# Performance work log

Hardware: AMD Instinct MI355X
Metric: run time of the kernel (lower is better)

The kernel has to match this reference:

```python
import jax, jax.numpy as jnp
import numpy as np

B = 262144
N_MAX = 4
N_EXPERTS = sum(n * n for n in range(1, N_MAX + 1))  # 30
# offset of expert block for each n (experts within n indexed by l*l + l + m)
OFFSETS = np.cumsum([0] + [n * n for n in range(1, N_MAX)])  # [0,1,5,14]


def _expert_id(n, l, m):
    off = jnp.asarray(OFFSETS, dtype=jnp.int32)
    return off[n - 1] + l * l + l + m  # (B,) int


def setup_inputs() -> dict:
    key = jax.random.key(0)
    ks = jax.random.split(key, 12)
    x = jax.random.normal(ks[0], (B, 3), dtype=jnp.float32)
    # valid coupled quantum numbers: 1<=n<=4, 0<=l<n, -l<=m<=l
    n = jax.random.randint(ks[1], (B,), 1, N_MAX + 1)
    ul = jax.random.uniform(ks[2], (B,))
    l = jnp.floor(ul * n.astype(jnp.float32)).astype(jnp.int32)
    l = jnp.clip(l, 0, n - 1)
    um = jax.random.uniform(ks[3], (B,))
    m = jnp.floor(um * (2 * l + 1).astype(jnp.float32)).astype(jnp.int32) - l
    m = jnp.clip(m, -l, l)
    s = 0.1
    W0 = jax.random.normal(ks[4], (3, 128), dtype=jnp.float32) * s
    b0 = jnp.zeros((128,), dtype=jnp.float32)
    W1 = jax.random.normal(ks[5], (128, 64), dtype=jnp.float32) * s
    b1 = jnp.zeros((64,), dtype=jnp.float32)
    Wa = jax.random.normal(ks[6], (N_EXPERTS, 64, 32), dtype=jnp.float32) * s
    ba = jax.random.normal(ks[7], (N_EXPERTS, 32), dtype=jnp.float32) * s
    Wb = jax.random.normal(ks[8], (N_EXPERTS, 32, 2), dtype=jnp.float32) * s
    bb = jax.random.normal(ks[9], (N_EXPERTS, 2), dtype=jnp.float32) * s
    return {"x": x, "n": n.astype(jnp.int32), "l": l, "m": m,
            "W0": W0, "b0": b0, "W1": W1, "b1": b1,
            "Wa": Wa, "ba": ba, "Wb": Wb, "bb": bb}


def reference(x, n, l, m, W0, b0, W1, b1, Wa, ba, Wb, bb):
    eid = _expert_id(n, l, m)  # (B,)
    # shared trunk (dropout is identity in eval mode)
    h = jnp.tanh(x @ W0 + b0)          # (B,128)
    h = jnp.tanh(h @ W1 + b1)          # (B,64)
    # per-sample expert dispatch via irregular gather of tiny MLP weights
    g = jnp.tanh(jnp.einsum('bd,bdh->bh', h, Wa[eid]) + ba[eid])  # (B,32)
    psi = jnp.einsum('bh,bho->bo', g, Wb[eid]) + bb[eid]          # (B,2)
    norm = jnp.sqrt(jnp.sum(psi * psi, axis=1, keepdims=True) + 1e-6)
    return psi / norm
```

## Files before the change

### kernel.cpp

```cpp
#include <hip/hip_runtime.h>
#include <math.h>


#define THREADS 64
#define NE 30
#define HB 256
#define PER 1024
#define MAXBLK 4126
#define SA 67
#define SG 36

typedef short bf16x8 __attribute__((ext_vector_type(8)));
typedef float f32x4 __attribute__((ext_vector_type(4)));

__device__ __forceinline__ int expert_id(int nn, int ll, int mm) {
    return ((nn - 1) * nn * (2 * nn - 1)) / 6 + ll * ll + ll + mm;
}

__device__ __forceinline__ float fast_tanh(float v) {
    float e = __builtin_exp2f(v * 2.885390082f);
    return fmaf(-2.0f, __builtin_amdgcn_rcpf(e + 1.0f), 1.0f);
}

__device__ __forceinline__ unsigned int f2b(float f) {
    unsigned int u = __float_as_uint(f);
    return (u + 0x7fffu + ((u >> 16) & 1u)) >> 16;
}
__device__ __forceinline__ float b2f(unsigned int b) {
    return __uint_as_float(b << 16);
}
__device__ __forceinline__ unsigned int packsplit(float v) {
    const unsigned int hb = f2b(v);
    const float lo = v - b2f(hb);
    return (__float_as_uint(lo) & 0xffff0000u) | hb;
}

union U8 { unsigned int u[4]; bf16x8 v; };
__device__ __forceinline__ void unpack8(const unsigned int* w, bf16x8& hi, bf16x8& lo) {
    U8 H, L;
#pragma unroll
    for (int i = 0; i < 4; ++i) {
        H.u[i] = __builtin_amdgcn_perm(w[2 * i + 1], w[2 * i], 0x05040100u);
        L.u[i] = __builtin_amdgcn_perm(w[2 * i + 1], w[2 * i], 0x07060302u);
    }
    hi = H.v; lo = L.v;
}

__global__ void hist_pack_kernel(const int* __restrict__ nq, const int* __restrict__ lq,
                                 const int* __restrict__ mq,
                                 int* __restrict__ eidr, int* __restrict__ cnt,
                                 const float* __restrict__ W1,
                                 unsigned short* __restrict__ W1fh, unsigned short* __restrict__ W1fl,
                                 const float* __restrict__ Wa,
                                 unsigned short* __restrict__ Wafh, unsigned short* __restrict__ Wafl,
                                 int B) {
    const int tid = threadIdx.x;
    const int bx = blockIdx.x;
    if (bx < HB) {
        __shared__ int h[NE];
        if (tid < NE) h[tid] = 0;
        __syncthreads();
        const int base = bx * PER;
        for (int i = tid; i < PER; i += blockDim.x) {
            const int e = expert_id(nq[base + i], lq[base + i], mq[base + i]);
            const int r = atomicAdd(&h[e], 1);
            eidr[base + i] = (r << 5) | e;
        }
        __syncthreads();
        if (tid < NE) cnt[bx * NE + tid] = h[tid];
    } else if (bx == HB) {
        for (int i = tid; i < 8192; i += blockDim.x) {
            const int j = i & 7, s = (i >> 3) & 15, q = (i >> 7) & 3;
            const int nt = (i >> 9) & 3, c = i >> 11;
            const int k = c * 32 + q * 8 + j, n = nt * 16 + s;
            const float w = W1[k * 64 + n];
            const unsigned int hb = f2b(w);
            W1fh[i] = (unsigned short)hb;
            W1fl[i] = (unsigned short)f2b(w - b2f(hb));
        }
    } else {
        const int e = bx - HB - 1;
        for (int i = tid; i < 2048; i += blockDim.x) {
            const int j = i & 7, s = (i >> 3) & 15, q = (i >> 7) & 3;
            const int nt2 = (i >> 9) & 1, c2 = (i >> 10) & 1;
            const int d = c2 * 32 + q * 8 + j, hh = nt2 * 16 + s;
            const float w = Wa[e * 2048 + d * 32 + hh];
            const unsigned int hb = f2b(w);
            Wafh[e * 2048 + i] = (unsigned short)hb;
            Wafl[e * 2048 + i] = (unsigned short)f2b(w - b2f(hb));
        }
    }
}

__global__ void scatter_kernel(const int* __restrict__ eidr, const int* __restrict__ cnt,
                               int* __restrict__ perm, int4* __restrict__ desc) {
    __shared__ int cl[HB * NE];
    __shared__ int bb[NE], tq[NE], esrt[NE + 1];
    const int tid = threadIdx.x;
    const int bx = blockIdx.x;
    for (int i = tid; i < HB * NE; i += blockDim.x) cl[i] = cnt[i];
    __syncthreads();
    if (tid < NE) {
        int s = 0, mybase = 0;
#pragma unroll 4
        for (int blk = 0; blk < HB; ++blk) {
            if (blk == bx) mybase = s;
            s += cl[blk * NE + tid];
        }
        bb[tid] = mybase;
        tq[tid] = s;
    }
    __syncthreads();
    if (tid == 0) {
        int es = 0;
        for (int e = 0; e < NE; ++e) { esrt[e] = es; es += tq[e]; }
        esrt[NE] = es;
    }
    __syncthreads();

    if (bx == HB) {
        __shared__ int pb[NE + 1];
        if (tid == 0) {
            int c = 0;
            for (int e = 0; e < NE; ++e) { pb[e] = c; c += (tq[e] + THREADS - 1) >> 6; }
            pb[NE] = c;
        }
        __syncthreads();
        const int tot = pb[NE];
        for (int b = tid; b < MAXBLK; b += blockDim.x) {
            int4 d = make_int4(-1, 0, 0, 0);
            if (b < tot) {
                int e = 0;
                while (pb[e + 1] <= b) ++e;
                const int seg = b - pb[e];
                d.x = e;
                d.y = esrt[e] + (seg << 6);
                d.z = min(THREADS, tq[e] - (seg << 6));
            }
            desc[b] = d;
        }
        return;
    }

    const int base = bx * PER;
    for (int i = tid; i < PER; i += blockDim.x) {
        const int p = eidr[base + i];
        const int e = p & 31;
        perm[esrt[e] + bb[e] + (p >> 5)] = base + i;
    }
}

__global__ __launch_bounds__(THREADS, 4) void wfc_kernel(
    const float* __restrict__ x, const int* __restrict__ perm,
    const int4* __restrict__ desc,
    const float* __restrict__ W0, const float* __restrict__ b0,
    const bf16x8* __restrict__ W1fh, const bf16x8* __restrict__ W1fl,
    const float* __restrict__ b1,
    const bf16x8* __restrict__ Wafh, const bf16x8* __restrict__ Wafl,
    const float* __restrict__ ba,
    const float* __restrict__ Wb, const float* __restrict__ bb,
    float* __restrict__ out)
{
    __shared__ unsigned int sbuf[2304];

    const int4 dsc = desc[blockIdx.x];
    if (dsc.x < 0) return;
    const int eid  = __builtin_amdgcn_readfirstlane(dsc.x);
    const int start = dsc.y;
    const int cnt   = dsc.z;

    const int tid = threadIdx.x;
    const bool valid = tid < cnt;
    const int idx = perm[start + (valid ? tid : 0)];

    const int lane = tid & 63;
    const int wv   = tid >> 6;
    const int qd   = lane >> 4;
    const int l16  = lane & 15;

    const float x0 = x[idx * 3 + 0];
    const float x1 = x[idx * 3 + 1];
    const float x2 = x[idx * 3 + 2];

    f32x4 acc[4][4];
#pragma unroll
    for (int nt = 0; nt < 4; ++nt) {
        const float bv = b1[nt * 16 + l16];
#pragma unroll
        for (int mt = 0; mt < 4; ++mt) {
            f32x4 c; c[0] = bv; c[1] = bv; c[2] = bv; c[3] = bv;
            acc[mt][nt] = c;
        }
    }

    for (int c = 0; c < 4; ++c) {
        if (c) __syncthreads();
#pragma unroll
        for (int kk = 0; kk < 32; ++kk) {
            const int k = c * 32 + kk;
            const float pre = fmaf(x0, W0[k], fmaf(x1, W0[128 + k], fmaf(x2, W0[256 + k], b0[k])));
            sbuf[kk * SA + tid] = packsplit(fast_tanh(pre));
        }
        __syncthreads();

        bf16x8 Bhi[4], Blo[4];
#pragma unroll
        for (int nt = 0; nt < 4; ++nt) {
            const int rec = (c * 4 + nt) * 64 + qd * 16 + l16;
            Bhi[nt] = W1fh[rec];
            Blo[nt] = W1fl[rec];
        }
#pragma unroll
        for (int mt = 0; mt < 4; ++mt) {
            unsigned int a[8];
            const int mrow = wv * 64 + mt * 16 + l16;
#pragma unroll
            for (int j = 0; j < 8; ++j) a[j] = sbuf[(qd * 8 + j) * SA + mrow];
            bf16x8 Ahi, Alo;
            unpack8(a, Ahi, Alo);
#pragma unroll
            for (int nt = 0; nt < 4; ++nt) {
                acc[mt][nt] = __builtin_amdgcn_mfma_f32_16x16x32_bf16(Ahi, Bhi[nt], acc[mt][nt], 0, 0, 0);
                acc[mt][nt] = __builtin_amdgcn_mfma_f32_16x16x32_bf16(Ahi, Blo[nt], acc[mt][nt], 0, 0, 0);
                acc[mt][nt] = __builtin_amdgcn_mfma_f32_16x16x32_bf16(Alo, Bhi[nt], acc[mt][nt], 0, 0, 0);
            }
        }
    }

    f32x4 acc2[4][2];
#pragma unroll
    for (int nt2 = 0; nt2 < 2; ++nt2) {
        const float bv = ba[(eid << 5) + nt2 * 16 + l16];
#pragma unroll
        for (int mt = 0; mt < 4; ++mt) {
            f32x4 c; c[0] = bv; c[1] = bv; c[2] = bv; c[3] = bv;
            acc2[mt][nt2] = c;
        }
    }

    const bf16x8* __restrict__ waeh = Wafh + (eid << 8);
    const bf16x8* __restrict__ wael = Wafl + (eid << 8);
    for (int c2 = 0; c2 < 2; ++c2) {
        __syncthreads();
#pragma unroll
        for (int mt = 0; mt < 4; ++mt) {
#pragma unroll
            for (int ntl = 0; ntl < 2; ++ntl) {
#pragma unroll
                for (int r = 0; r < 4; ++r) {
                    const float h2 = fast_tanh(acc[mt][c2 * 2 + ntl][r]);
                    const int dl  = ntl * 16 + l16;
                    const int row = wv * 64 + mt * 16 + qd * 4 + r;
                    sbuf[dl * SA + row] = packsplit(h2);
                }
            }
        }
        __syncthreads();

        bf16x8 B2hi[2], B2lo[2];
#pragma unroll
        for (int nt2 = 0; nt2 < 2; ++nt2) {
            const int rec = (c2 * 2 + nt2) * 64 + qd * 16 + l16;
            B2hi[nt2] = waeh[rec];
            B2lo[nt2] = wael[rec];
        }
#pragma unroll
        for (int mt = 0; mt < 4; ++mt) {
            unsigned int a[8];
            const int mrow = wv * 64 + mt * 16 + l16;
#pragma unroll
            for (int j = 0; j < 8; ++j) a[j] = sbuf[(qd * 8 + j) * SA + mrow];
            bf16x8 Ahi, Alo;
            unpack8(a, Ahi, Alo);
#pragma unroll
            for (int nt2 = 0; nt2 < 2; ++nt2) {
                acc2[mt][nt2] = __builtin_amdgcn_mfma_f32_16x16x32_bf16(Ahi, B2hi[nt2], acc2[mt][nt2], 0, 0, 0);
                acc2[mt][nt2] = __builtin_amdgcn_mfma_f32_16x16x32_bf16(Ahi, B2lo[nt2], acc2[mt][nt2], 0, 0, 0);
                acc2[mt][nt2] = __builtin_amdgcn_mfma_f32_16x16x32_bf16(Alo, B2hi[nt2], acc2[mt][nt2], 0, 0, 0);
            }
        }
    }

    __syncthreads();
    float* g2 = (float*)sbuf;
#pragma unroll
    for (int mt = 0; mt < 4; ++mt) {
#pragma unroll
        for (int nt2 = 0; nt2 < 2; ++nt2) {
#pragma unroll
            for (int r = 0; r < 4; ++r) {
                const int row = wv * 64 + mt * 16 + qd * 4 + r;
                g2[row * SG + nt2 * 16 + l16] = fast_tanh(acc2[mt][nt2][r]);
            }
        }
    }
    __syncthreads();

    float gv[32];
    {
        const float4* grow = (const float4*)(g2 + tid * SG);
#pragma unroll
        for (int i = 0; i < 8; ++i) {
            float4 v = grow[i];
            gv[4 * i + 0] = v.x; gv[4 * i + 1] = v.y;
            gv[4 * i + 2] = v.z; gv[4 * i + 3] = v.w;
        }
    }

    const float* __restrict__ wbe = Wb + (eid << 6);
    float p0 = bb[2 * eid], p1 = bb[2 * eid + 1];
#pragma unroll
    for (int h = 0; h < 32; ++h) {
        p0 = fmaf(gv[h], wbe[2 * h + 0], p0);
        p1 = fmaf(gv[h], wbe[2 * h + 1], p1);
    }

    const float s = fmaf(p0, p0, fmaf(p1, p1, 1e-6f));
    const float inv = 1.0f / sqrtf(s);
    if (valid) {
        float2 o; o.x = p0 * inv; o.y = p1 * inv;
        ((float2*)out)[idx] = o;
    }
}

extern "C" void kernel_launch(void* const* d_in, const int* in_sizes, int n_in,
                              void* d_out, int out_size, void* d_ws, size_t ws_size,
                              hipStream_t stream) {
    const float* x  = (const float*)d_in[0];
    const int*   n  = (const int*)d_in[1];
    const int*   l  = (const int*)d_in[2];
    const int*   m  = (const int*)d_in[3];
    const float* W0 = (const float*)d_in[4];
    const float* b0 = (const float*)d_in[5];
    const float* W1 = (const float*)d_in[6];
    const float* b1 = (const float*)d_in[7];
    const float* Wa = (const float*)d_in[8];
    const float* ba = (const float*)d_in[9];
    const float* Wb = (const float*)d_in[10];
    const float* bb = (const float*)d_in[11];
    float* out = (float*)d_out;

    const int B = in_sizes[1];

    int*            perm  = (int*)d_ws;
    int*            eidr  = perm + B;
    int*            cnt   = eidr + B;
    int4*           desc  = (int4*)(cnt + HB * NE);
    unsigned short* W1fh  = (unsigned short*)(desc + MAXBLK);
    unsigned short* W1fl  = W1fh + 8192;
    unsigned short* Wafh  = W1fl + 8192;
    unsigned short* Wafl  = Wafh + NE * 2048;

    hist_pack_kernel<<<HB + 1 + NE, 256, 0, stream>>>(
        n, l, m, eidr, cnt, W1, W1fh, W1fl, Wa, Wafh, Wafl, B);
    scatter_kernel<<<HB + 1, 256, 0, stream>>>(eidr, cnt, perm, desc);
    wfc_kernel<<<MAXBLK, THREADS, 0, stream>>>(
        x, perm, desc, W0, b0,
        (const bf16x8*)W1fh, (const bf16x8*)W1fl, b1,
        (const bf16x8*)Wafh, (const bf16x8*)Wafl, ba, Wb, bb, out);
}
```

Baseline: 156.8 us.

## Fuse histogram and scatter into one kernel with a grid-wide spin barrier

Merges the histogram and scatter kernels into one prologue kernel. Blocks publish their per-expert counts and then spin on a global atomic counter until all 256 histogram blocks have arrived. Each block keeps its packed ranks in registers instead of writing them to global memory and reading them back. The per-block descriptor table is dropped, and each main-kernel block now finds its expert segment by scanning the 30 expert totals. This removes one kernel launch and a global round trip, but relies on all 256 blocks being co-resident and adds a memset plus per-block scan work.

```diff
diff --git a/kernel.cpp b/kernel.cpp
--- a/kernel.cpp
+++ b/kernel.cpp
@@ -46,28 +46,78 @@
     hi = H.v; lo = L.v;
 }
 
-__global__ void hist_pack_kernel(const int* __restrict__ nq, const int* __restrict__ lq,
-                                 const int* __restrict__ mq,
-                                 int* __restrict__ eidr, int* __restrict__ cnt,
-                                 const float* __restrict__ W1,
-                                 unsigned short* __restrict__ W1fh, unsigned short* __restrict__ W1fl,
-                                 const float* __restrict__ Wa,
-                                 unsigned short* __restrict__ Wafh, unsigned short* __restrict__ Wafl,
-                                 int B) {
+__global__ void fused_prologue(const int* __restrict__ nq, const int* __restrict__ lq,
+                               const int* __restrict__ mq,
+                               int* __restrict__ cnt, int* __restrict__ done,
+                               int* __restrict__ etot, int* __restrict__ perm,
+                               const float* __restrict__ W1,
+                               unsigned short* __restrict__ W1fh, unsigned short* __restrict__ W1fl,
+                               const float* __restrict__ Wa,
+                               unsigned short* __restrict__ Wafh, unsigned short* __restrict__ Wafl,
+                               int B) {
     const int tid = threadIdx.x;
     const int bx = blockIdx.x;
+
     if (bx < HB) {
         __shared__ int h[NE];
+        __shared__ int cl[HB * NE];
+        __shared__ int bb[NE], tq[NE], esrt[NE];
         if (tid < NE) h[tid] = 0;
         __syncthreads();
+
         const int base = bx * PER;
-        for (int i = tid; i < PER; i += blockDim.x) {
-            const int e = expert_id(nq[base + i], lq[base + i], mq[base + i]);
+        int pk[4];
+#pragma unroll
+        for (int j = 0; j < 4; ++j) {
+            const int i = base + tid + j * 256;
+            const int e = expert_id(nq[i], lq[i], mq[i]);
             const int r = atomicAdd(&h[e], 1);
-            eidr[base + i] = (r << 5) | e;
-        }
-        __syncthreads();
-        if (tid < NE) cnt[bx * NE + tid] = h[tid];
+            pk[j] = (r << 5) | e;
+        }
+        __syncthreads();
+
+        if (tid < NE)
+            __hip_atomic_store(&cnt[bx * NE + tid], h[tid],
+                               __ATOMIC_RELEASE, __HIP_MEMORY_SCOPE_AGENT);
+        __syncthreads();
+        if (tid == 0) {
+            __threadfence();
+            atomicAdd(done, 1);
+            while (__hip_atomic_load(done, __ATOMIC_ACQUIRE,
+                                     __HIP_MEMORY_SCOPE_AGENT) < HB) {
+                __builtin_amdgcn_s_sleep(8);
+            }
+        }
+        __syncthreads();
+
+        for (int i = tid; i < HB * NE; i += 256)
+            cl[i] = __hip_atomic_load(&cnt[i], __ATOMIC_RELAXED,
+                                      __HIP_MEMORY_SCOPE_AGENT);
+        __syncthreads();
+
+        if (tid < NE) {
+            int s = 0, mybase = 0;
+#pragma unroll 4
+            for (int blk = 0; blk < HB; ++blk) {
+                if (blk == bx) mybase = s;
+                s += cl[blk * NE + tid];
+            }
+            bb[tid] = mybase;
+            tq[tid] = s;
+        }
+        __syncthreads();
+        if (tid == 0) {
+            int es = 0;
+            for (int e = 0; e < NE; ++e) { esrt[e] = es; es += tq[e]; }
+        }
+        __syncthreads();
+        if (bx == 0 && tid < NE) etot[tid] = tq[tid];
+
+#pragma unroll
+        for (int j = 0; j < 4; ++j) {
+            const int e = pk[j] & 31;
+            perm[esrt[e] + bb[e] + (pk[j] >> 5)] = base + tid + j * 256;
+        }
     } else if (bx == HB) {
         for (int i = tid; i < 8192; i += blockDim.x) {
             const int j = i & 7, s = (i >> 3) & 15, q = (i >> 7) & 3;
@@ -92,67 +142,9 @@
     }
 }
 
-__global__ void scatter_kernel(const int* __restrict__ eidr, const int* __restrict__ cnt,
-                               int* __restrict__ perm, int4* __restrict__ desc) {
-    __shared__ int cl[HB * NE];
-    __shared__ int bb[NE], tq[NE], esrt[NE + 1];
-    const int tid = threadIdx.x;
-    const int bx = blockIdx.x;
-    for (int i = tid; i < HB * NE; i += blockDim.x) cl[i] = cnt[i];
-    __syncthreads();
-    if (tid < NE) {
-        int s = 0, mybase = 0;
-#pragma unroll 4
-        for (int blk = 0; blk < HB; ++blk) {
-            if (blk == bx) mybase = s;
-            s += cl[blk * NE + tid];
-        }
-        bb[tid] = mybase;
-        tq[tid] = s;
-    }
-    __syncthreads();
-    if (tid == 0) {
-        int es = 0;
-        for (int e = 0; e < NE; ++e) { esrt[e] = es; es += tq[e]; }
-        esrt[NE] = es;
-    }
-    __syncthreads();
-
-    if (bx == HB) {
-        __shared__ int pb[NE + 1];
-        if (tid == 0) {
-            int c = 0;
-            for (int e = 0; e < NE; ++e) { pb[e] = c; c += (tq[e] + THREADS - 1) >> 6; }
-            pb[NE] = c;
-        }
-        __syncthreads();
-        const int tot = pb[NE];
-        for (int b = tid; b < MAXBLK; b += blockDim.x) {
-            int4 d = make_int4(-1, 0, 0, 0);
-            if (b < tot) {
-                int e = 0;
-                while (pb[e + 1] <= b) ++e;
-                const int seg = b - pb[e];
-                d.x = e;
-                d.y = esrt[e] + (seg << 6);
-                d.z = min(THREADS, tq[e] - (seg << 6));
-            }
-            desc[b] = d;
-        }
-        return;
-    }
-
-    const int base = bx * PER;
-    for (int i = tid; i < PER; i += blockDim.x) {
-        const int p = eidr[base + i];
-        const int e = p & 31;
-        perm[esrt[e] + bb[e] + (p >> 5)] = base + i;
-    }
-}
-
 __global__ __launch_bounds__(THREADS, 4) void wfc_kernel(
     const float* __restrict__ x, const int* __restrict__ perm,
-    const int4* __restrict__ desc,
+    const int* __restrict__ etot,
     const float* __restrict__ W0, const float* __restrict__ b0,
     const bf16x8* __restrict__ W1fh, const bf16x8* __restrict__ W1fl,
     const float* __restrict__ b1,
@@ -163,11 +155,23 @@
 {
     __shared__ unsigned int sbuf[2304];
 
-    const int4 dsc = desc[blockIdx.x];
-    if (dsc.x < 0) return;
-    const int eid  = __builtin_amdgcn_readfirstlane(dsc.x);
-    const int start = dsc.y;
-    const int cnt   = dsc.z;
+    int eid = -1, start = 0, cnt = 0;
+    {
+        int cum = 0, es = 0;
+#pragma unroll 1
+        for (int e = 0; e < NE; ++e) {
+            const int t = etot[e];
+            const int nb = (t + 63) >> 6;
+            if ((int)blockIdx.x < cum + nb) {
+                const int seg = blockIdx.x - cum;
+                eid = e; start = es + (seg << 6); cnt = min(64, t - (seg << 6));
+                break;
+            }
+            cum += nb; es += t;
+        }
+    }
+    if (eid < 0) return;
+    eid = __builtin_amdgcn_readfirstlane(eid);
 
     const int tid = threadIdx.x;
     const bool valid = tid < cnt;
@@ -342,20 +346,20 @@
 
     const int B = in_sizes[1];
 
-    int*            perm  = (int*)d_ws;
-    int*            eidr  = perm + B;
-    int*            cnt   = eidr + B;
-    int4*           desc  = (int4*)(cnt + HB * NE);
-    unsigned short* W1fh  = (unsigned short*)(desc + MAXBLK);
+    int*            done  = (int*)d_ws;
+    int*            cnt   = done + 32;
+    int*            etot  = cnt + HB * NE;
+    int*            perm  = etot + 32;
+    unsigned short* W1fh  = (unsigned short*)(perm + B);
     unsigned short* W1fl  = W1fh + 8192;
     unsigned short* Wafh  = W1fl + 8192;
     unsigned short* Wafl  = Wafh + NE * 2048;
 
-    hist_pack_kernel<<<HB + 1 + NE, 256, 0, stream>>>(
-        n, l, m, eidr, cnt, W1, W1fh, W1fl, Wa, Wafh, Wafl, B);
-    scatter_kernel<<<HB + 1, 256, 0, stream>>>(eidr, cnt, perm, desc);
+    hipMemsetAsync(done, 0, sizeof(int), stream);
+    fused_prologue<<<HB + 1 + NE, 256, 0, stream>>>(
+        n, l, m, cnt, done, etot, perm, W1, W1fh, W1fl, Wa, Wafh, Wafl, B);
     wfc_kernel<<<MAXBLK, THREADS, 0, stream>>>(
-        x, perm, desc, W0, b0,
+        x, perm, etot, W0, b0,
         (const bf16x8*)W1fh, (const bf16x8*)W1fl, b1,
         (const bf16x8*)Wafh, (const bf16x8*)Wafl, ba, Wb, bb, out);
 }
```

After: 158.6 us. No clear change (+1.2%).
